# Optimization experiments

Hardware: AMD Instinct MI355X
Metric: run time of the kernel (lower is better)

## Reference

```python
import jax, jax.numpy as jnp
import numpy as np

NUM_SKILLS = 1000
DIM_S = 64
SIZE_M = 64
B, T = 64, 200


def setup_inputs() -> dict:
    key = jax.random.key(0)
    ks = jax.random.split(key, 16)
    skills = jax.random.randint(ks[0], (B, T), 0, NUM_SKILLS)
    responses = jax.random.randint(ks[1], (B, T), 0, 2)
    s = 1.0 / np.sqrt(DIM_S)
    return {
        "skills": skills,
        "responses": responses,
        "k_emb": jax.random.normal(ks[2], (NUM_SKILLS, DIM_S)) * s,
        "v_emb": jax.random.normal(ks[3], (2 * NUM_SKILLS, DIM_S)) * s,
        "Mk": jax.random.normal(ks[4], (SIZE_M, DIM_S)) * np.sqrt(2.0 / DIM_S),
        "Mv0": jax.random.normal(ks[5], (SIZE_M, DIM_S)) * np.sqrt(2.0 / DIM_S),
        "fW": jax.random.normal(ks[6], (DIM_S, 2 * DIM_S)) * (1.0 / np.sqrt(2 * DIM_S)),
        "fb": jnp.zeros((DIM_S,)),
        "eW": jax.random.normal(ks[7], (DIM_S, DIM_S)) * s,
        "eb": jnp.zeros((DIM_S,)),
        "aW": jax.random.normal(ks[8], (DIM_S, DIM_S)) * s,
        "ab": jnp.zeros((DIM_S,)),
        "pW": jax.random.normal(ks[9], (1, DIM_S)) * s,
        "pb": jnp.zeros((1,)),
    }


def reference(skills, responses, k_emb, v_emb, Mk, Mv0, fW, fb, eW, eb, aW, ab, pW, pb):
    # dropout is identity in eval mode
    masked_r = responses * (responses > -1).astype(responses.dtype)
    x = skills + NUM_SKILLS * masked_r            # [B, T]
    k = k_emb[skills]                              # [B, T, D]
    v = v_emb[x]                                   # [B, T, D]
    w = jax.nn.softmax(jnp.einsum('btd,md->btm', k, Mk), axis=-1)  # [B, T, M]
    e = jax.nn.sigmoid(v @ eW.T + eb)              # [B, T, D]
    a = jnp.tanh(v @ aW.T + ab)                    # [B, T, D]

    Mv_init = jnp.broadcast_to(Mv0, (skills.shape[0],) + Mv0.shape)  # [B, M, D]

    def step(Mvt, inp):
        wt, et, at = inp                           # [B,M], [B,D], [B,D]
        read = jnp.einsum('bm,bmd->bd', wt, Mvt)   # read BEFORE update (Mv[:, :-1])
        Mvt = Mvt * (1.0 - wt[:, :, None] * et[:, None, :]) + wt[:, :, None] * at[:, None, :]
        return Mvt, read

    xs = (jnp.swapaxes(w, 0, 1), jnp.swapaxes(e, 0, 1), jnp.swapaxes(a, 0, 1))
    _, reads = jax.lax.scan(step, Mv_init, xs)     # reads: [T, B, D]
    reads = jnp.swapaxes(reads, 0, 1)              # [B, T, D]

    f = jnp.tanh(jnp.concatenate([reads, k], axis=-1) @ fW.T + fb)  # [B, T, D]
    p = jax.nn.sigmoid(f @ pW.T + pb)[..., 0]      # [B, T]
    return p[:, 1:]                                # pred, [B, T-1]
```

## Files before the change

### kernel.cpp

```cpp
#include <hip/hip_runtime.h>
#include <hip/hip_bf16.h>
#include <stdint.h>

#define NSK 1000
#define TT  200
#define BB  64
#define NROW (BB * TT)
#define NOUT (BB * (TT-1))
#define CH  8
#define RW  8

__device__ __forceinline__ float lane_bcast(float v, int l) {
  return __uint_as_float(__builtin_amdgcn_readlane(__float_as_uint(v), l));
}
__device__ __forceinline__ unsigned ulane_bcast(unsigned v, int l) {
  return __builtin_amdgcn_readlane(v, l);
}
__device__ __forceinline__ float frcp(float x) { return __builtin_amdgcn_rcpf(x); }
__device__ __forceinline__ float sigm(float x) { return frcp(1.f + __expf(-x)); }
__device__ __forceinline__ float tanh_fast(float x) {
  return fmaf(-2.f, frcp(1.f + __expf(2.f * x)), 1.f);
}

typedef _Float16 half2v __attribute__((ext_vector_type(2)));
union H2U { unsigned u; half2v h; };
__device__ __forceinline__ unsigned pack2h(float a, float b) {
  H2U x; x.h = (half2v){(_Float16)a, (_Float16)b}; return x.u;
}
__device__ __forceinline__ float dot2h(unsigned sp, unsigned wp, float acc) {
#if __has_builtin(__builtin_amdgcn_fdot2)
  H2U s, w; s.u = sp; w.u = wp;
  return __builtin_amdgcn_fdot2(s.h, w.h, acc, false);
#else
  H2U s, w; s.u = sp; w.u = wp;
  return fmaf((float)s.h.y, (float)w.h.y, fmaf((float)s.h.x, (float)w.h.x, acc));
#endif
}
__device__ __forceinline__ unsigned pack_pairs(float v) {
  const int lane = threadIdx.x & 63;
  float a = __shfl(v, 2 * lane);
  float b = __shfl(v, 2 * lane + 1);
  return pack2h(a, b);
}

__global__ __launch_bounds__(256) void wea_kernel(
    const int* __restrict__ skills, const int* __restrict__ responses,
    const float* __restrict__ k_emb, const float* __restrict__ v_emb,
    const float* __restrict__ Mk, const float* __restrict__ eW,
    const float* __restrict__ eb, const float* __restrict__ aW,
    const float* __restrict__ ab,
    float* __restrict__ w_ws, float* __restrict__ e_ws, float* __restrict__ a_ws)
{
  __shared__ unsigned sw[3 * 64 * 40];
  const int tid = threadIdx.x;
  for (int ch = tid; ch < 1536; ch += 256) {
    const int mat = ch >> 9;
    const int rem = ch & 511;
    const int j = rem >> 3, cc = rem & 7;
    const float4* src = (mat == 0) ? (const float4*)Mk
                      : (mat == 1) ? (const float4*)eW : (const float4*)aW;
    const float4 f0 = src[j * 16 + cc * 2];
    const float4 f1 = src[j * 16 + cc * 2 + 1];
    uint4 pk;
    pk.x = pack2h(f0.x, f0.y); pk.y = pack2h(f0.z, f0.w);
    pk.z = pack2h(f1.x, f1.y); pk.w = pack2h(f1.z, f1.w);
    *(uint4*)&sw[mat * 2560 + j * 40 + ((cc + j) & 7) * 4] = pk;
  }
  __syncthreads();

  const int wave = tid >> 6, lane = tid & 63;
  const float ebl = eb[lane], abl = ab[lane];
  const int r0 = (blockIdx.x * 4 + wave) * 2;

  float kv[2], vv[2];
  #pragma unroll
  for (int i = 0; i < 2; ++i) {
    const int sk = skills[r0 + i];
    int rr = responses[r0 + i]; rr = (rr > -1) ? rr : 0;
    kv[i] = k_emb[(size_t)sk * 64 + lane];
    vv[i] = v_emb[(size_t)(sk + NSK * rr) * 64 + lane];
  }
  unsigned kp[2], vp[2];
  #pragma unroll
  for (int i = 0; i < 2; ++i) { kp[i] = pack_pairs(kv[i]); vp[i] = pack_pairs(vv[i]); }

  float accK[2] = {0.f, 0.f}, accE[2] = {0.f, 0.f}, accA[2] = {0.f, 0.f};
  #pragma unroll 1
  for (int h = 0; h < 2; ++h) {
    uint4 qm[4], qe[4], qa[4];
    #pragma unroll
    for (int c = 0; c < 4; ++c) {
      const int off = lane * 40 + (((h * 4 + c) + lane) & 7) * 4;
      qm[c] = *(const uint4*)&sw[off];
      qe[c] = *(const uint4*)&sw[2560 + off];
      qa[c] = *(const uint4*)&sw[5120 + off];
    }
    #pragma unroll
    for (int i = 0; i < 2; ++i) {
      #pragma unroll
      for (int c = 0; c < 4; ++c) {
        const unsigned um[4] = {qm[c].x, qm[c].y, qm[c].z, qm[c].w};
        const unsigned ue[4] = {qe[c].x, qe[c].y, qe[c].z, qe[c].w};
        const unsigned ua[4] = {qa[c].x, qa[c].y, qa[c].z, qa[c].w};
        #pragma unroll
        for (int m = 0; m < 4; ++m) {
          const int idx = (h * 4 + c) * 4 + m;
          const unsigned spk = ulane_bcast(kp[i], idx);
          const unsigned spv = ulane_bcast(vp[i], idx);
          accK[i] = dot2h(spk, um[m], accK[i]);
          accE[i] = dot2h(spv, ue[m], accE[i]);
          accA[i] = dot2h(spv, ua[m], accA[i]);
        }
      }
    }
  }

  #pragma unroll
  for (int i = 0; i < 2; ++i) {
    const int row = r0 + i;
    float mx = accK[i];
    #pragma unroll
    for (int off = 32; off; off >>= 1) mx = fmaxf(mx, __shfl_xor(mx, off));
    float ex = __expf(accK[i] - mx);
    float sm = ex;
    #pragma unroll
    for (int off = 32; off; off >>= 1) sm += __shfl_xor(sm, off);
    w_ws[(size_t)row * 64 + lane] = ex * frcp(sm);
    e_ws[(size_t)row * 64 + lane] = sigm(accE[i] + ebl);
    a_ws[(size_t)row * 64 + lane] = tanh_fast(accA[i] + abl);
  }
}

__device__ __forceinline__ void load_chunk(
    const float* __restrict__ wr, const float* __restrict__ er,
    const float* __restrict__ ar, int t0, int wl, int lane,
    float* wb, float* ebf, float* abf)
{
  #pragma unroll
  for (int k = 0; k < CH; ++k) {
    wb[k]  = wr[(t0 + k) * 64 + wl];
    ebf[k] = er[(t0 + k) * 64 + lane];
    abf[k] = ar[(t0 + k) * 64 + lane];
  }
}

__device__ __forceinline__ void compute_chunk(
    float* Mv, const float* wb, const float* ebf, const float* abf,
    float* __restrict__ red, int wave, int lane)
{
  #pragma unroll
  for (int k = 0; k < CH; ++k) {
    const float wv = wb[k], ev = ebf[k], av = abf[k];
    float rp = 0.f;
    #pragma unroll
    for (int i = 0; i < RW; ++i) {
      float wm = lane_bcast(wv, i);
      rp = fmaf(wm, Mv[i], rp);
      float tp = fmaf(-ev, Mv[i], av);
      Mv[i] = fmaf(wm, tp, Mv[i]);
    }
    red[k * 256 + wave * 64 + lane] = rp;
  }
}

__device__ __forceinline__ void reduce_store(
    const float* __restrict__ red, int ch, int b, int s, int wave, int lane,
    float* __restrict__ part_ws)
{
  #pragma unroll
  for (int u = 0; u < 2; ++u) {
    const float* rr = red + (wave * 2 + u) * 256;
    const float v = (rr[lane] + rr[64 + lane]) + (rr[128 + lane] + rr[192 + lane]);
    const int t = ch * CH + wave * 2 + u;
    part_ws[((size_t)b * TT + t) * 128 + s * 64 + lane] = v;
  }
}

__global__ __launch_bounds__(256) void scan_kernel(
    const float* __restrict__ Mv0,
    const float* __restrict__ w_ws, const float* __restrict__ e_ws,
    const float* __restrict__ a_ws, float* __restrict__ part_ws)
{
  __shared__ float red[2][CH * 256];
  const int b    = blockIdx.x >> 1;
  const int s    = blockIdx.x & 1;
  const int wave = threadIdx.x >> 6;
  const int lane = threadIdx.x & 63;
  const int m0   = s * 32 + wave * RW;
  const int wl   = m0 + (lane & (RW - 1));
  float Mv[RW];
  #pragma unroll
  for (int i = 0; i < RW; ++i) Mv[i] = Mv0[(size_t)(m0 + i) * 64 + lane];

  const float* wr = w_ws + (size_t)b * TT * 64;
  const float* er = e_ws + (size_t)b * TT * 64;
  const float* ar = a_ws + (size_t)b * TT * 64;

  float wb0[CH], eb0[CH], ab0[CH];
  float wb1[CH], eb1[CH], ab1[CH];
  load_chunk(wr, er, ar, 0, wl, lane, wb0, eb0, ab0);
  for (int ch = 0; ch < TT / CH; ch += 2) {
    if ((ch + 1) * CH < TT)
      load_chunk(wr, er, ar, (ch + 1) * CH, wl, lane, wb1, eb1, ab1);
    compute_chunk(Mv, wb0, eb0, ab0, red[0], wave, lane);
    __syncthreads();
    reduce_store(red[0], ch, b, s, wave, lane, part_ws);
    if ((ch + 2) * CH < TT)
      load_chunk(wr, er, ar, (ch + 2) * CH, wl, lane, wb0, eb0, ab0);
    if ((ch + 1) * CH < TT) {
      compute_chunk(Mv, wb1, eb1, ab1, red[1], wave, lane);
      __syncthreads();
      reduce_store(red[1], ch + 1, b, s, wave, lane, part_ws);
    }
  }
}

__global__ __launch_bounds__(256) void fp_kernel(
    const int* __restrict__ skills, const float* __restrict__ k_emb,
    const float* __restrict__ fW, const float* __restrict__ fb,
    const float* __restrict__ pW, const float* __restrict__ pb,
    const float* __restrict__ part_ws, float* __restrict__ out)
{
  __shared__ unsigned sf[64 * 72];
  const int tid = threadIdx.x;
  for (int ch = tid; ch < 1024; ch += 256) {
    const int j = ch >> 4, cc = ch & 15;
    const float4 f0 = ((const float4*)fW)[j * 32 + cc * 2];
    const float4 f1 = ((const float4*)fW)[j * 32 + cc * 2 + 1];
    uint4 pk;
    pk.x = pack2h(f0.x, f0.y); pk.y = pack2h(f0.z, f0.w);
    pk.z = pack2h(f1.x, f1.y); pk.w = pack2h(f1.z, f1.w);
    *(uint4*)&sf[j * 72 + ((cc + j) & 15) * 4] = pk;
  }
  __syncthreads();

  const int wave = tid >> 6, lane = tid & 63;
  const float fbl = fb[lane], pwl = pW[lane], pb0 = pb[0];
  const int p = blockIdx.x * 4 + wave;

  float pc[2][2], kc[2];
  int bsave[2], tsave[2];
  #pragma unroll
  for (int i = 0; i < 2; ++i) {
    const unsigned idx = 2u * p + i;
    const unsigned b = idx / 199u;
    const int row = (int)(idx + b + 1u);
    bsave[i] = (int)b; tsave[i] = (int)(idx - b * 199u);
    const float* pp = part_ws + (size_t)row * 128;
    pc[i][0] = pp[lane]; pc[i][1] = pp[64 + lane];
    kc[i] = k_emb[(size_t)skills[row] * 64 + lane];
  }
  unsigned rvp[2], kvp[2];
  #pragma unroll
  for (int i = 0; i < 2; ++i) {
    rvp[i] = pack_pairs(pc[i][0] + pc[i][1]);
    kvp[i] = pack_pairs(kc[i]);
  }

  float acc[2] = {fbl, fbl};
  #pragma unroll 1
  for (int h = 0; h < 4; ++h) {
    uint4 qf[4];
    #pragma unroll
    for (int c = 0; c < 4; ++c)
      qf[c] = *(const uint4*)&sf[lane * 72 + (((h * 4 + c) + lane) & 15) * 4];
    #pragma unroll
    for (int i = 0; i < 2; ++i) {
      #pragma unroll
      for (int c = 0; c < 4; ++c) {
        const unsigned uu[4] = {qf[c].x, qf[c].y, qf[c].z, qf[c].w};
        #pragma unroll
        for (int m = 0; m < 4; ++m) {
          const int idx = (h * 4 + c) * 4 + m;
          const unsigned sp = (idx < 32) ? ulane_bcast(rvp[i], idx)
                                         : ulane_bcast(kvp[i], idx - 32);
          acc[i] = dot2h(sp, uu[m], acc[i]);
        }
      }
    }
  }

  float f0 = tanh_fast(acc[0]) * pwl;
  float f1 = tanh_fast(acc[1]) * pwl;
  #pragma unroll
  for (int off = 32; off; off >>= 1) {
    f0 += __shfl_xor(f0, off);
    f1 += __shfl_xor(f1, off);
  }
  if (lane == 0) {
    out[(size_t)bsave[0] * (TT - 1) + tsave[0]] = sigm(f0 + pb0);
    out[(size_t)bsave[1] * (TT - 1) + tsave[1]] = sigm(f1 + pb0);
  }
}

extern "C" void kernel_launch(void* const* d_in, const int* in_sizes, int n_in,
                              void* d_out, int out_size, void* d_ws, size_t ws_size,
                              hipStream_t stream) {
  const int* skills    = (const int*)d_in[0];
  const int* responses = (const int*)d_in[1];
  const float* k_emb   = (const float*)d_in[2];
  const float* v_emb   = (const float*)d_in[3];
  const float* Mk      = (const float*)d_in[4];
  const float* Mv0     = (const float*)d_in[5];
  const float* fW      = (const float*)d_in[6];
  const float* fb      = (const float*)d_in[7];
  const float* eW      = (const float*)d_in[8];
  const float* eb      = (const float*)d_in[9];
  const float* aW      = (const float*)d_in[10];
  const float* ab      = (const float*)d_in[11];
  const float* pW      = (const float*)d_in[12];
  const float* pb      = (const float*)d_in[13];

  float* w_ws    = (float*)d_ws;
  float* e_ws    = w_ws + (size_t)BB * TT * 64;
  float* a_ws    = e_ws + (size_t)BB * TT * 64;
  float* part_ws = a_ws + (size_t)BB * TT * 64;

  wea_kernel<<<dim3(NROW / 8), 256, 0, stream>>>(
      skills, responses, k_emb, v_emb, Mk, eW, eb, aW, ab, w_ws, e_ws, a_ws);
  scan_kernel<<<dim3(BB * 2), 256, 0, stream>>>(Mv0, w_ws, e_ws, a_ws, part_ws);
  fp_kernel<<<dim3(NOUT / 8), 256, 0, stream>>>(
      skills, k_emb, fW, fb, pW, pb, part_ws, (float*)d_out);
}
```

Measured before the change: 135.2 us.

## Fuse three stages into one persistent kernel with per-batch atomic counters

Merges the projection, recurrent scan and output-projection kernels into a single launch whose blocks are split by role: 800 blocks produce w/e/a and bump per-batch counters, 128 scan blocks spin on those counters, and the first 796 producer blocks later wait on scan counters to compute outputs. This removes two kernel launch boundaries and lets scans for finished batches start while other batches are still being projected. Each producer block now handles 16 rows instead of 8. It risks deadlock if scan blocks are resident while producers cannot be scheduled, and adds a memset plus spin-wait overhead.

```diff
diff --git a/kernel.cpp b/kernel.cpp
--- a/kernel.cpp
+++ b/kernel.cpp
@@ -9,6 +9,10 @@
 #define NOUT (BB * (TT-1))
 #define CH  8
 #define RW  8
+#define NW  800
+#define NS  128
+#define NFP 796
+#define NBLK (NW + NS)
 
 __device__ __forceinline__ float lane_bcast(float v, int l) {
   return __uint_as_float(__builtin_amdgcn_readlane(__float_as_uint(v), l));
@@ -43,92 +47,9 @@
   return pack2h(a, b);
 }
 
-__global__ __launch_bounds__(256) void wea_kernel(
-    const int* __restrict__ skills, const int* __restrict__ responses,
-    const float* __restrict__ k_emb, const float* __restrict__ v_emb,
-    const float* __restrict__ Mk, const float* __restrict__ eW,
-    const float* __restrict__ eb, const float* __restrict__ aW,
-    const float* __restrict__ ab,
-    float* __restrict__ w_ws, float* __restrict__ e_ws, float* __restrict__ a_ws)
-{
-  __shared__ unsigned sw[3 * 64 * 40];
-  const int tid = threadIdx.x;
-  for (int ch = tid; ch < 1536; ch += 256) {
-    const int mat = ch >> 9;
-    const int rem = ch & 511;
-    const int j = rem >> 3, cc = rem & 7;
-    const float4* src = (mat == 0) ? (const float4*)Mk
-                      : (mat == 1) ? (const float4*)eW : (const float4*)aW;
-    const float4 f0 = src[j * 16 + cc * 2];
-    const float4 f1 = src[j * 16 + cc * 2 + 1];
-    uint4 pk;
-    pk.x = pack2h(f0.x, f0.y); pk.y = pack2h(f0.z, f0.w);
-    pk.z = pack2h(f1.x, f1.y); pk.w = pack2h(f1.z, f1.w);
-    *(uint4*)&sw[mat * 2560 + j * 40 + ((cc + j) & 7) * 4] = pk;
-  }
-  __syncthreads();
-
-  const int wave = tid >> 6, lane = tid & 63;
-  const float ebl = eb[lane], abl = ab[lane];
-  const int r0 = (blockIdx.x * 4 + wave) * 2;
-
-  float kv[2], vv[2];
-  #pragma unroll
-  for (int i = 0; i < 2; ++i) {
-    const int sk = skills[r0 + i];
-    int rr = responses[r0 + i]; rr = (rr > -1) ? rr : 0;
-    kv[i] = k_emb[(size_t)sk * 64 + lane];
-    vv[i] = v_emb[(size_t)(sk + NSK * rr) * 64 + lane];
-  }
-  unsigned kp[2], vp[2];
-  #pragma unroll
-  for (int i = 0; i < 2; ++i) { kp[i] = pack_pairs(kv[i]); vp[i] = pack_pairs(vv[i]); }
-
-  float accK[2] = {0.f, 0.f}, accE[2] = {0.f, 0.f}, accA[2] = {0.f, 0.f};
-  #pragma unroll 1
-  for (int h = 0; h < 2; ++h) {
-    uint4 qm[4], qe[4], qa[4];
-    #pragma unroll
-    for (int c = 0; c < 4; ++c) {
-      const int off = lane * 40 + (((h * 4 + c) + lane) & 7) * 4;
-      qm[c] = *(const uint4*)&sw[off];
-      qe[c] = *(const uint4*)&sw[2560 + off];
-      qa[c] = *(const uint4*)&sw[5120 + off];
-    }
-    #pragma unroll
-    for (int i = 0; i < 2; ++i) {
-      #pragma unroll
-      for (int c = 0; c < 4; ++c) {
-        const unsigned um[4] = {qm[c].x, qm[c].y, qm[c].z, qm[c].w};
-        const unsigned ue[4] = {qe[c].x, qe[c].y, qe[c].z, qe[c].w};
-        const unsigned ua[4] = {qa[c].x, qa[c].y, qa[c].z, qa[c].w};
-        #pragma unroll
-        for (int m = 0; m < 4; ++m) {
-          const int idx = (h * 4 + c) * 4 + m;
-          const unsigned spk = ulane_bcast(kp[i], idx);
-          const unsigned spv = ulane_bcast(vp[i], idx);
-          accK[i] = dot2h(spk, um[m], accK[i]);
-          accE[i] = dot2h(spv, ue[m], accE[i]);
-          accA[i] = dot2h(spv, ua[m], accA[i]);
-        }
-      }
-    }
-  }
-
-  #pragma unroll
-  for (int i = 0; i < 2; ++i) {
-    const int row = r0 + i;
-    float mx = accK[i];
-    #pragma unroll
-    for (int off = 32; off; off >>= 1) mx = fmaxf(mx, __shfl_xor(mx, off));
-    float ex = __expf(accK[i] - mx);
-    float sm = ex;
-    #pragma unroll
-    for (int off = 32; off; off >>= 1) sm += __shfl_xor(sm, off);
-    w_ws[(size_t)row * 64 + lane] = ex * frcp(sm);
-    e_ws[(size_t)row * 64 + lane] = sigm(accE[i] + ebl);
-    a_ws[(size_t)row * 64 + lane] = tanh_fast(accA[i] + abl);
-  }
+__device__ __forceinline__ void spin_ge(unsigned* p, unsigned tgt) {
+  while (__hip_atomic_load(p, __ATOMIC_RELAXED, __HIP_MEMORY_SCOPE_AGENT) < tgt)
+    __builtin_amdgcn_s_sleep(8);
 }
 
 __device__ __forceinline__ void load_chunk(
@@ -176,120 +97,230 @@
   }
 }
 
-__global__ __launch_bounds__(256) void scan_kernel(
-    const float* __restrict__ Mv0,
-    const float* __restrict__ w_ws, const float* __restrict__ e_ws,
-    const float* __restrict__ a_ws, float* __restrict__ part_ws)
+__global__ __launch_bounds__(256, 4) void dkvmn_pipe(
+    const int* __restrict__ skills, const int* __restrict__ responses,
+    const float* __restrict__ k_emb, const float* __restrict__ v_emb,
+    const float* __restrict__ Mk, const float* __restrict__ Mv0,
+    const float* __restrict__ fW, const float* __restrict__ fb,
+    const float* __restrict__ eW, const float* __restrict__ eb,
+    const float* __restrict__ aW, const float* __restrict__ ab,
+    const float* __restrict__ pW, const float* __restrict__ pb,
+    unsigned* __restrict__ wcnt, unsigned* __restrict__ scnt,
+    float* __restrict__ w_ws, float* __restrict__ e_ws, float* __restrict__ a_ws,
+    float* __restrict__ part_ws, float* __restrict__ out)
 {
-  __shared__ float red[2][CH * 256];
-  const int b    = blockIdx.x >> 1;
-  const int s    = blockIdx.x & 1;
-  const int wave = threadIdx.x >> 6;
-  const int lane = threadIdx.x & 63;
-  const int m0   = s * 32 + wave * RW;
-  const int wl   = m0 + (lane & (RW - 1));
-  float Mv[RW];
-  #pragma unroll
-  for (int i = 0; i < RW; ++i) Mv[i] = Mv0[(size_t)(m0 + i) * 64 + lane];
-
-  const float* wr = w_ws + (size_t)b * TT * 64;
-  const float* er = e_ws + (size_t)b * TT * 64;
-  const float* ar = a_ws + (size_t)b * TT * 64;
-
-  float wb0[CH], eb0[CH], ab0[CH];
-  float wb1[CH], eb1[CH], ab1[CH];
-  load_chunk(wr, er, ar, 0, wl, lane, wb0, eb0, ab0);
-  for (int ch = 0; ch < TT / CH; ch += 2) {
-    if ((ch + 1) * CH < TT)
-      load_chunk(wr, er, ar, (ch + 1) * CH, wl, lane, wb1, eb1, ab1);
-    compute_chunk(Mv, wb0, eb0, ab0, red[0], wave, lane);
+  __shared__ unsigned smem[7680];
+  const int tid = threadIdx.x;
+  const int wave = tid >> 6, lane = tid & 63;
+
+  if (blockIdx.x >= NW) {
+    const int j = blockIdx.x - NW, b = j >> 1, s = j & 1;
+    if (tid == 0) { spin_ge(&wcnt[b], 200u); __threadfence(); }
     __syncthreads();
-    reduce_store(red[0], ch, b, s, wave, lane, part_ws);
-    if ((ch + 2) * CH < TT)
-      load_chunk(wr, er, ar, (ch + 2) * CH, wl, lane, wb0, eb0, ab0);
-    if ((ch + 1) * CH < TT) {
-      compute_chunk(Mv, wb1, eb1, ab1, red[1], wave, lane);
+
+    const int m0 = s * 32 + wave * RW;
+    const int wl = m0 + (lane & (RW - 1));
+    float Mv[RW];
+    #pragma unroll
+    for (int i = 0; i < RW; ++i) Mv[i] = Mv0[(size_t)(m0 + i) * 64 + lane];
+
+    const float* wr = w_ws + (size_t)b * TT * 64;
+    const float* er = e_ws + (size_t)b * TT * 64;
+    const float* ar = a_ws + (size_t)b * TT * 64;
+    float* red0 = (float*)smem;
+    float* red1 = red0 + CH * 256;
+
+    float wb0[CH], eb0[CH], ab0[CH];
+    float wb1[CH], eb1[CH], ab1[CH];
+    load_chunk(wr, er, ar, 0, wl, lane, wb0, eb0, ab0);
+    for (int ch = 0; ch < TT / CH; ch += 2) {
+      if ((ch + 1) * CH < TT)
+        load_chunk(wr, er, ar, (ch + 1) * CH, wl, lane, wb1, eb1, ab1);
+      compute_chunk(Mv, wb0, eb0, ab0, red0, wave, lane);
       __syncthreads();
-      reduce_store(red[1], ch + 1, b, s, wave, lane, part_ws);
-    }
-  }
-}
-
-__global__ __launch_bounds__(256) void fp_kernel(
-    const int* __restrict__ skills, const float* __restrict__ k_emb,
-    const float* __restrict__ fW, const float* __restrict__ fb,
-    const float* __restrict__ pW, const float* __restrict__ pb,
-    const float* __restrict__ part_ws, float* __restrict__ out)
-{
-  __shared__ unsigned sf[64 * 72];
-  const int tid = threadIdx.x;
-  for (int ch = tid; ch < 1024; ch += 256) {
-    const int j = ch >> 4, cc = ch & 15;
-    const float4 f0 = ((const float4*)fW)[j * 32 + cc * 2];
-    const float4 f1 = ((const float4*)fW)[j * 32 + cc * 2 + 1];
+      reduce_store(red0, ch, b, s, wave, lane, part_ws);
+      if ((ch + 2) * CH < TT)
+        load_chunk(wr, er, ar, (ch + 2) * CH, wl, lane, wb0, eb0, ab0);
+      if ((ch + 1) * CH < TT) {
+        compute_chunk(Mv, wb1, eb1, ab1, red1, wave, lane);
+        __syncthreads();
+        reduce_store(red1, ch + 1, b, s, wave, lane, part_ws);
+      }
+    }
+    __syncthreads();
+    if (tid == 0) {
+      __threadfence();
+      __hip_atomic_fetch_add(&scnt[b], 1u, __ATOMIC_RELEASE, __HIP_MEMORY_SCOPE_AGENT);
+    }
+    return;
+  }
+
+  for (int ch = tid; ch < 1536; ch += 256) {
+    const int mat = ch >> 9, rem = ch & 511;
+    const int j = rem >> 3, cc = rem & 7;
+    const float4* src = (mat == 0) ? (const float4*)Mk
+                      : (mat == 1) ? (const float4*)eW : (const float4*)aW;
+    const float4 f0 = src[j * 16 + cc * 2];
+    const float4 f1 = src[j * 16 + cc * 2 + 1];
     uint4 pk;
     pk.x = pack2h(f0.x, f0.y); pk.y = pack2h(f0.z, f0.w);
     pk.z = pack2h(f1.x, f1.y); pk.w = pack2h(f1.z, f1.w);
-    *(uint4*)&sf[j * 72 + ((cc + j) & 15) * 4] = pk;
+    *(uint4*)&smem[mat * 2560 + j * 40 + ((cc + j) & 7) * 4] = pk;
   }
   __syncthreads();
-
-  const int wave = tid >> 6, lane = tid & 63;
-  const float fbl = fb[lane], pwl = pW[lane], pb0 = pb[0];
-  const int p = blockIdx.x * 4 + wave;
-
-  float pc[2][2], kc[2];
-  int bsave[2], tsave[2];
-  #pragma unroll
-  for (int i = 0; i < 2; ++i) {
-    const unsigned idx = 2u * p + i;
-    const unsigned b = idx / 199u;
-    const int row = (int)(idx + b + 1u);
-    bsave[i] = (int)b; tsave[i] = (int)(idx - b * 199u);
-    const float* pp = part_ws + (size_t)row * 128;
-    pc[i][0] = pp[lane]; pc[i][1] = pp[64 + lane];
-    kc[i] = k_emb[(size_t)skills[row] * 64 + lane];
-  }
-  unsigned rvp[2], kvp[2];
-  #pragma unroll
-  for (int i = 0; i < 2; ++i) {
-    rvp[i] = pack_pairs(pc[i][0] + pc[i][1]);
-    kvp[i] = pack_pairs(kc[i]);
-  }
-
-  float acc[2] = {fbl, fbl};
-  #pragma unroll 1
-  for (int h = 0; h < 4; ++h) {
-    uint4 qf[4];
-    #pragma unroll
-    for (int c = 0; c < 4; ++c)
-      qf[c] = *(const uint4*)&sf[lane * 72 + (((h * 4 + c) + lane) & 15) * 4];
-    #pragma unroll
-    for (int i = 0; i < 2; ++i) {
+  {
+    const float ebl = eb[lane], abl = ab[lane];
+    const int r0 = blockIdx.x * 16 + wave * 4;
+
+    float kv[4], vv[4];
+    #pragma unroll
+    for (int i = 0; i < 4; ++i) {
+      const int sk = skills[r0 + i];
+      int rr = responses[r0 + i]; rr = (rr > -1) ? rr : 0;
+      kv[i] = k_emb[(size_t)sk * 64 + lane];
+      vv[i] = v_emb[(size_t)(sk + NSK * rr) * 64 + lane];
+    }
+    unsigned kp[4], vp[4];
+    #pragma unroll
+    for (int i = 0; i < 4; ++i) { kp[i] = pack_pairs(kv[i]); vp[i] = pack_pairs(vv[i]); }
+
+    float accK[4] = {0,0,0,0}, accE[4] = {0,0,0,0}, accA[4] = {0,0,0,0};
+    #pragma unroll 1
+    for (int h = 0; h < 2; ++h) {
+      uint4 qm[4], qe[4], qa[4];
       #pragma unroll
       for (int c = 0; c < 4; ++c) {
-        const unsigned uu[4] = {qf[c].x, qf[c].y, qf[c].z, qf[c].w};
+        const int off = lane * 40 + (((h * 4 + c) + lane) & 7) * 4;
+        qm[c] = *(const uint4*)&smem[off];
+        qe[c] = *(const uint4*)&smem[2560 + off];
+        qa[c] = *(const uint4*)&smem[5120 + off];
+      }
+      #pragma unroll
+      for (int i = 0; i < 4; ++i) {
         #pragma unroll
-        for (int m = 0; m < 4; ++m) {
-          const int idx = (h * 4 + c) * 4 + m;
-          const unsigned sp = (idx < 32) ? ulane_bcast(rvp[i], idx)
-                                         : ulane_bcast(kvp[i], idx - 32);
-          acc[i] = dot2h(sp, uu[m], acc[i]);
+        for (int c = 0; c < 4; ++c) {
+          const unsigned um[4] = {qm[c].x, qm[c].y, qm[c].z, qm[c].w};
+          const unsigned ue[4] = {qe[c].x, qe[c].y, qe[c].z, qe[c].w};
+          const unsigned ua[4] = {qa[c].x, qa[c].y, qa[c].z, qa[c].w};
+          #pragma unroll
+          for (int m = 0; m < 4; ++m) {
+            const int idx = (h * 4 + c) * 4 + m;
+            const unsigned spk = ulane_bcast(kp[i], idx);
+            const unsigned spv = ulane_bcast(vp[i], idx);
+            accK[i] = dot2h(spk, um[m], accK[i]);
+            accE[i] = dot2h(spv, ue[m], accE[i]);
+            accA[i] = dot2h(spv, ua[m], accA[i]);
+          }
         }
       }
     }
-  }
-
-  float f0 = tanh_fast(acc[0]) * pwl;
-  float f1 = tanh_fast(acc[1]) * pwl;
-  #pragma unroll
-  for (int off = 32; off; off >>= 1) {
-    f0 += __shfl_xor(f0, off);
-    f1 += __shfl_xor(f1, off);
-  }
-  if (lane == 0) {
-    out[(size_t)bsave[0] * (TT - 1) + tsave[0]] = sigm(f0 + pb0);
-    out[(size_t)bsave[1] * (TT - 1) + tsave[1]] = sigm(f1 + pb0);
+    #pragma unroll
+    for (int i = 0; i < 4; ++i) {
+      const int row = r0 + i;
+      float mx = accK[i];
+      #pragma unroll
+      for (int off = 32; off; off >>= 1) mx = fmaxf(mx, __shfl_xor(mx, off));
+      float ex = __expf(accK[i] - mx);
+      float sm = ex;
+      #pragma unroll
+      for (int off = 32; off; off >>= 1) sm += __shfl_xor(sm, off);
+      w_ws[(size_t)row * 64 + lane] = ex * frcp(sm);
+      e_ws[(size_t)row * 64 + lane] = sigm(accE[i] + ebl);
+      a_ws[(size_t)row * 64 + lane] = tanh_fast(accA[i] + abl);
+    }
+  }
+  __syncthreads();
+  if (tid == 0) {
+    __threadfence();
+    const int r0 = blockIdx.x * 16;
+    const int b0 = r0 / TT, b1 = (r0 + 15) / TT;
+    if (b0 == b1) {
+      __hip_atomic_fetch_add(&wcnt[b0], 16u, __ATOMIC_RELEASE, __HIP_MEMORY_SCOPE_AGENT);
+    } else {
+      const unsigned n0 = (unsigned)((b0 + 1) * TT - r0);
+      __hip_atomic_fetch_add(&wcnt[b0], n0, __ATOMIC_RELEASE, __HIP_MEMORY_SCOPE_AGENT);
+      __hip_atomic_fetch_add(&wcnt[b1], 16u - n0, __ATOMIC_RELEASE, __HIP_MEMORY_SCOPE_AGENT);
+    }
+  }
+
+  if (blockIdx.x >= NFP) return;
+
+  {
+    const int idx0 = blockIdx.x * 16, idx1 = idx0 + 15;
+    const int bf = idx0 / 199, bl = idx1 / 199;
+    if (tid == 0) {
+      spin_ge(&scnt[bf], 2u);
+      if (bl != bf) spin_ge(&scnt[bl], 2u);
+      __threadfence();
+    }
+    __syncthreads();
+    for (int ch = tid; ch < 1024; ch += 256) {
+      const int j = ch >> 4, cc = ch & 15;
+      const float4 f0 = ((const float4*)fW)[j * 32 + cc * 2];
+      const float4 f1 = ((const float4*)fW)[j * 32 + cc * 2 + 1];
+      uint4 pk;
+      pk.x = pack2h(f0.x, f0.y); pk.y = pack2h(f0.z, f0.w);
+      pk.z = pack2h(f1.x, f1.y); pk.w = pack2h(f1.z, f1.w);
+      *(uint4*)&smem[j * 72 + ((cc + j) & 15) * 4] = pk;
+    }
+    __syncthreads();
+
+    const float fbl = fb[lane], pwl = pW[lane], pb0 = pb[0];
+    #pragma unroll 1
+    for (int pi = 0; pi < 2; ++pi) {
+      const int p = blockIdx.x * 8 + wave * 2 + pi;
+      float pc[2][2], kc[2];
+      int bsave[2], tsave[2];
+      #pragma unroll
+      for (int i = 0; i < 2; ++i) {
+        const unsigned idx = 2u * p + i;
+        const unsigned b = idx / 199u;
+        const int row = (int)(idx + b + 1u);
+        bsave[i] = (int)b; tsave[i] = (int)(idx - b * 199u);
+        const float* pp = part_ws + (size_t)row * 128;
+        pc[i][0] = pp[lane]; pc[i][1] = pp[64 + lane];
+        kc[i] = k_emb[(size_t)skills[row] * 64 + lane];
+      }
+      unsigned rvp[2], kvp[2];
+      #pragma unroll
+      for (int i = 0; i < 2; ++i) {
+        rvp[i] = pack_pairs(pc[i][0] + pc[i][1]);
+        kvp[i] = pack_pairs(kc[i]);
+      }
+      float acc[2] = {fbl, fbl};
+      #pragma unroll 1
+      for (int h = 0; h < 4; ++h) {
+        uint4 qf[4];
+        #pragma unroll
+        for (int c = 0; c < 4; ++c)
+          qf[c] = *(const uint4*)&smem[lane * 72 + (((h * 4 + c) + lane) & 15) * 4];
+        #pragma unroll
+        for (int i = 0; i < 2; ++i) {
+          #pragma unroll
+          for (int c = 0; c < 4; ++c) {
+            const unsigned uu[4] = {qf[c].x, qf[c].y, qf[c].z, qf[c].w};
+            #pragma unroll
+            for (int m = 0; m < 4; ++m) {
+              const int idx = (h * 4 + c) * 4 + m;
+              const unsigned sp = (idx < 32) ? ulane_bcast(rvp[i], idx)
+                                             : ulane_bcast(kvp[i], idx - 32);
+              acc[i] = dot2h(sp, uu[m], acc[i]);
+            }
+          }
+        }
+      }
+      float f0 = tanh_fast(acc[0]) * pwl;
+      float f1 = tanh_fast(acc[1]) * pwl;
+      #pragma unroll
+      for (int off = 32; off; off >>= 1) {
+        f0 += __shfl_xor(f0, off);
+        f1 += __shfl_xor(f1, off);
+      }
+      if (lane == 0) {
+        out[(size_t)bsave[0] * (TT - 1) + tsave[0]] = sigm(f0 + pb0);
+        out[(size_t)bsave[1] * (TT - 1) + tsave[1]] = sigm(f1 + pb0);
+      }
+    }
   }
 }
 
@@ -311,14 +342,16 @@
   const float* pW      = (const float*)d_in[12];
   const float* pb      = (const float*)d_in[13];
 
-  float* w_ws    = (float*)d_ws;
+  unsigned* wcnt = (unsigned*)d_ws;
+  unsigned* scnt = wcnt + 64;
+  float* base    = (float*)d_ws + 256;
+  float* w_ws    = base;
   float* e_ws    = w_ws + (size_t)BB * TT * 64;
   float* a_ws    = e_ws + (size_t)BB * TT * 64;
   float* part_ws = a_ws + (size_t)BB * TT * 64;
 
-  wea_kernel<<<dim3(NROW / 8), 256, 0, stream>>>(
-      skills, responses, k_emb, v_emb, Mk, eW, eb, aW, ab, w_ws, e_ws, a_ws);
-  scan_kernel<<<dim3(BB * 2), 256, 0, stream>>>(Mv0, w_ws, e_ws, a_ws, part_ws);
-  fp_kernel<<<dim3(NOUT / 8), 256, 0, stream>>>(
-      skills, k_emb, fW, fb, pW, pb, part_ws, (float*)d_out);
-}
+  hipMemsetAsync(d_ws, 0, 1024, stream);
+  dkvmn_pipe<<<dim3(NBLK), dim3(256), 0, stream>>>(
+      skills, responses, k_emb, v_emb, Mk, Mv0, fW, fb, eW, eb, aW, ab, pW, pb,
+      wcnt, scnt, w_ws, e_ws, a_ws, part_ws, (float*)d_out);
+}
```

Measured after the change: 207.7 us. +53.6%, slower.

## Fuse memory scan and output projection into one per-batch kernel

Applied to the files above, without the earlier changes.

Merges the scan kernel and the final projection kernel into a single kernel with one 512-thread block per batch row. Each block holds all 64 memory slots, so the cross-block partial-read sum goes away, and the block then runs the fW/pW projection over its own reads. This drops a kernel launch and the partial-sum round trip, but cuts the scan grid from 128 to 64 blocks. The projection phase is also limited to 64 blocks, which lowers parallelism on a GPU with many compute units.

```diff
diff --git a/kernel.cpp b/kernel.cpp
--- a/kernel.cpp
+++ b/kernel.cpp
@@ -6,7 +6,6 @@
 #define TT  200
 #define BB  64
 #define NROW (BB * TT)
-#define NOUT (BB * (TT-1))
 #define CH  8
 #define RW  8
 
@@ -54,8 +53,7 @@
   __shared__ unsigned sw[3 * 64 * 40];
   const int tid = threadIdx.x;
   for (int ch = tid; ch < 1536; ch += 256) {
-    const int mat = ch >> 9;
-    const int rem = ch & 511;
+    const int mat = ch >> 9, rem = ch & 511;
     const int j = rem >> 3, cc = rem & 7;
     const float4* src = (mat == 0) ? (const float4*)Mk
                       : (mat == 1) ? (const float4*)eW : (const float4*)aW;
@@ -114,7 +112,6 @@
       }
     }
   }
-
   #pragma unroll
   for (int i = 0; i < 2; ++i) {
     const int row = r0 + i;
@@ -159,137 +156,113 @@
       float tp = fmaf(-ev, Mv[i], av);
       Mv[i] = fmaf(wm, tp, Mv[i]);
     }
-    red[k * 256 + wave * 64 + lane] = rp;
-  }
-}
-
-__device__ __forceinline__ void reduce_store(
-    const float* __restrict__ red, int ch, int b, int s, int wave, int lane,
-    float* __restrict__ part_ws)
-{
-  #pragma unroll
-  for (int u = 0; u < 2; ++u) {
-    const float* rr = red + (wave * 2 + u) * 256;
-    const float v = (rr[lane] + rr[64 + lane]) + (rr[128 + lane] + rr[192 + lane]);
-    const int t = ch * CH + wave * 2 + u;
-    part_ws[((size_t)b * TT + t) * 128 + s * 64 + lane] = v;
-  }
-}
-
-__global__ __launch_bounds__(256) void scan_kernel(
+    red[k * 512 + wave * 64 + lane] = rp;
+  }
+}
+
+__global__ __launch_bounds__(512) void sfp_kernel(
+    const int* __restrict__ skills, const float* __restrict__ k_emb,
     const float* __restrict__ Mv0,
-    const float* __restrict__ w_ws, const float* __restrict__ e_ws,
-    const float* __restrict__ a_ws, float* __restrict__ part_ws)
-{
-  __shared__ float red[2][CH * 256];
-  const int b    = blockIdx.x >> 1;
-  const int s    = blockIdx.x & 1;
-  const int wave = threadIdx.x >> 6;
-  const int lane = threadIdx.x & 63;
-  const int m0   = s * 32 + wave * RW;
-  const int wl   = m0 + (lane & (RW - 1));
-  float Mv[RW];
-  #pragma unroll
-  for (int i = 0; i < RW; ++i) Mv[i] = Mv0[(size_t)(m0 + i) * 64 + lane];
-
-  const float* wr = w_ws + (size_t)b * TT * 64;
-  const float* er = e_ws + (size_t)b * TT * 64;
-  const float* ar = a_ws + (size_t)b * TT * 64;
-
-  float wb0[CH], eb0[CH], ab0[CH];
-  float wb1[CH], eb1[CH], ab1[CH];
-  load_chunk(wr, er, ar, 0, wl, lane, wb0, eb0, ab0);
-  for (int ch = 0; ch < TT / CH; ch += 2) {
-    if ((ch + 1) * CH < TT)
-      load_chunk(wr, er, ar, (ch + 1) * CH, wl, lane, wb1, eb1, ab1);
-    compute_chunk(Mv, wb0, eb0, ab0, red[0], wave, lane);
-    __syncthreads();
-    reduce_store(red[0], ch, b, s, wave, lane, part_ws);
-    if ((ch + 2) * CH < TT)
-      load_chunk(wr, er, ar, (ch + 2) * CH, wl, lane, wb0, eb0, ab0);
-    if ((ch + 1) * CH < TT) {
-      compute_chunk(Mv, wb1, eb1, ab1, red[1], wave, lane);
-      __syncthreads();
-      reduce_store(red[1], ch + 1, b, s, wave, lane, part_ws);
-    }
-  }
-}
-
-__global__ __launch_bounds__(256) void fp_kernel(
-    const int* __restrict__ skills, const float* __restrict__ k_emb,
     const float* __restrict__ fW, const float* __restrict__ fb,
     const float* __restrict__ pW, const float* __restrict__ pb,
-    const float* __restrict__ part_ws, float* __restrict__ out)
-{
-  __shared__ unsigned sf[64 * 72];
+    const float* __restrict__ w_ws, const float* __restrict__ e_ws,
+    const float* __restrict__ a_ws,
+    float* __restrict__ read_ws, float* __restrict__ out)
+{
+  __shared__ float sred[2][CH * 512];
+  __shared__ unsigned sfw[64 * 72];
   const int tid = threadIdx.x;
-  for (int ch = tid; ch < 1024; ch += 256) {
+  const int wave = tid >> 6, lane = tid & 63;
+  const int b = blockIdx.x, base = b * TT;
+
+  for (int ch = tid; ch < 1024; ch += 512) {
     const int j = ch >> 4, cc = ch & 15;
     const float4 f0 = ((const float4*)fW)[j * 32 + cc * 2];
     const float4 f1 = ((const float4*)fW)[j * 32 + cc * 2 + 1];
     uint4 pk;
     pk.x = pack2h(f0.x, f0.y); pk.y = pack2h(f0.z, f0.w);
     pk.z = pack2h(f1.x, f1.y); pk.w = pack2h(f1.z, f1.w);
-    *(uint4*)&sf[j * 72 + ((cc + j) & 15) * 4] = pk;
-  }
+    *(uint4*)&sfw[j * 72 + ((cc + j) & 15) * 4] = pk;
+  }
+
+  const int m0 = wave * RW;
+  const int wl = m0 + (lane & (RW - 1));
+  float Mv[RW];
+  #pragma unroll
+  for (int i = 0; i < RW; ++i) Mv[i] = Mv0[(size_t)(m0 + i) * 64 + lane];
+  const float* wr = w_ws + (size_t)base * 64;
+  const float* er = e_ws + (size_t)base * 64;
+  const float* ar = a_ws + (size_t)base * 64;
+
+  float wb0[CH], eb0[CH], ab0[CH];
+  float wb1[CH], eb1[CH], ab1[CH];
+  load_chunk(wr, er, ar, 0, wl, lane, wb0, eb0, ab0);
   __syncthreads();
 
-  const int wave = tid >> 6, lane = tid & 63;
+  for (int c = 0; c < TT / CH; ++c) {
+    if (c + 1 < TT / CH) {
+      if (c & 1) load_chunk(wr, er, ar, (c + 1) * CH, wl, lane, wb0, eb0, ab0);
+      else       load_chunk(wr, er, ar, (c + 1) * CH, wl, lane, wb1, eb1, ab1);
+    }
+    float* red = sred[c & 1];
+    if (c & 1) compute_chunk(Mv, wb1, eb1, ab1, red, wave, lane);
+    else       compute_chunk(Mv, wb0, eb0, ab0, red, wave, lane);
+    __syncthreads();
+    const float* r = red + wave * 512;
+    float v = ((r[0 * 64 + lane] + r[1 * 64 + lane]) + (r[2 * 64 + lane] + r[3 * 64 + lane]))
+            + ((r[4 * 64 + lane] + r[5 * 64 + lane]) + (r[6 * 64 + lane] + r[7 * 64 + lane]));
+    read_ws[(size_t)(base + c * CH + wave) * 64 + lane] = v;
+  }
+  __threadfence_block();
+  __syncthreads();
+
   const float fbl = fb[lane], pwl = pW[lane], pb0 = pb[0];
-  const int p = blockIdx.x * 4 + wave;
-
-  float pc[2][2], kc[2];
-  int bsave[2], tsave[2];
-  #pragma unroll
-  for (int i = 0; i < 2; ++i) {
-    const unsigned idx = 2u * p + i;
-    const unsigned b = idx / 199u;
-    const int row = (int)(idx + b + 1u);
-    bsave[i] = (int)b; tsave[i] = (int)(idx - b * 199u);
-    const float* pp = part_ws + (size_t)row * 128;
-    pc[i][0] = pp[lane]; pc[i][1] = pp[64 + lane];
-    kc[i] = k_emb[(size_t)skills[row] * 64 + lane];
-  }
-  unsigned rvp[2], kvp[2];
-  #pragma unroll
-  for (int i = 0; i < 2; ++i) {
-    rvp[i] = pack_pairs(pc[i][0] + pc[i][1]);
-    kvp[i] = pack_pairs(kc[i]);
-  }
-
-  float acc[2] = {fbl, fbl};
   #pragma unroll 1
-  for (int h = 0; h < 4; ++h) {
-    uint4 qf[4];
-    #pragma unroll
-    for (int c = 0; c < 4; ++c)
-      qf[c] = *(const uint4*)&sf[lane * 72 + (((h * 4 + c) + lane) & 15) * 4];
-    #pragma unroll
-    for (int i = 0; i < 2; ++i) {
-      #pragma unroll
-      for (int c = 0; c < 4; ++c) {
-        const unsigned uu[4] = {qf[c].x, qf[c].y, qf[c].z, qf[c].w};
+  for (int g0 = 0; g0 < 25; g0 += 5) {
+    float rv[5], kc[5];
+    int ov[5];
+    #pragma unroll
+    for (int i = 0; i < 5; ++i) {
+      const int o = wave * 25 + g0 + i;
+      ov[i] = o;
+      const int t = (o < TT - 1) ? o + 1 : TT - 1;
+      rv[i] = read_ws[(size_t)(base + t) * 64 + lane];
+      kc[i] = k_emb[(size_t)skills[base + t] * 64 + lane];
+    }
+    unsigned rvp[5], kvp[5];
+    #pragma unroll
+    for (int i = 0; i < 5; ++i) { rvp[i] = pack_pairs(rv[i]); kvp[i] = pack_pairs(kc[i]); }
+
+    float acc[5] = {fbl, fbl, fbl, fbl, fbl};
+    #pragma unroll 1
+    for (int h = 0; h < 4; ++h) {
+      uint4 qf[4];
+      #pragma unroll
+      for (int c = 0; c < 4; ++c)
+        qf[c] = *(const uint4*)&sfw[lane * 72 + (((h * 4 + c) + lane) & 15) * 4];
+      #pragma unroll
+      for (int i = 0; i < 5; ++i) {
         #pragma unroll
-        for (int m = 0; m < 4; ++m) {
-          const int idx = (h * 4 + c) * 4 + m;
-          const unsigned sp = (idx < 32) ? ulane_bcast(rvp[i], idx)
-                                         : ulane_bcast(kvp[i], idx - 32);
-          acc[i] = dot2h(sp, uu[m], acc[i]);
+        for (int c = 0; c < 4; ++c) {
+          const unsigned uu[4] = {qf[c].x, qf[c].y, qf[c].z, qf[c].w};
+          #pragma unroll
+          for (int m = 0; m < 4; ++m) {
+            const int idx = (h * 4 + c) * 4 + m;
+            const unsigned sp = (idx < 32) ? ulane_bcast(rvp[i], idx)
+                                           : ulane_bcast(kvp[i], idx - 32);
+            acc[i] = dot2h(sp, uu[m], acc[i]);
+          }
         }
       }
     }
-  }
-
-  float f0 = tanh_fast(acc[0]) * pwl;
-  float f1 = tanh_fast(acc[1]) * pwl;
-  #pragma unroll
-  for (int off = 32; off; off >>= 1) {
-    f0 += __shfl_xor(f0, off);
-    f1 += __shfl_xor(f1, off);
-  }
-  if (lane == 0) {
-    out[(size_t)bsave[0] * (TT - 1) + tsave[0]] = sigm(f0 + pb0);
-    out[(size_t)bsave[1] * (TT - 1) + tsave[1]] = sigm(f1 + pb0);
+    #pragma unroll
+    for (int i = 0; i < 5; ++i) {
+      float f = tanh_fast(acc[i]) * pwl;
+      #pragma unroll
+      for (int off = 32; off; off >>= 1) f += __shfl_xor(f, off);
+      if (lane == 0 && ov[i] < TT - 1)
+        out[(size_t)b * (TT - 1) + ov[i]] = sigm(f + pb0);
+    }
   }
 }
 
@@ -314,11 +287,11 @@
   float* w_ws    = (float*)d_ws;
   float* e_ws    = w_ws + (size_t)BB * TT * 64;
   float* a_ws    = e_ws + (size_t)BB * TT * 64;
-  float* part_ws = a_ws + (size_t)BB * TT * 64;
+  float* read_ws = a_ws + (size_t)BB * TT * 64;
 
   wea_kernel<<<dim3(NROW / 8), 256, 0, stream>>>(
       skills, responses, k_emb, v_emb, Mk, eW, eb, aW, ab, w_ws, e_ws, a_ws);
-  scan_kernel<<<dim3(BB * 2), 256, 0, stream>>>(Mv0, w_ws, e_ws, a_ws, part_ws);
-  fp_kernel<<<dim3(NOUT / 8), 256, 0, stream>>>(
-      skills, k_emb, fW, fb, pW, pb, part_ws, (float*)d_out);
-}
+  sfp_kernel<<<dim3(BB), 512, 0, stream>>>(
+      skills, k_emb, Mv0, fW, fb, pW, pb, w_ws, e_ws, a_ws,
+      read_ws, (float*)d_out);
+}
```

Measured after the change: 198.4 us. 1.47x slower.

## Store intermediates as fp16 and enlarge scan chunk to cut memory traffic

Applied to the files above, without the earlier changes.

The w/e/a workspaces are now written in half precision, with e and a packed together into one 32-bit word and w in 16-bit. The scan's partial read outputs are split into two fp16 arrays, one per half-block. The scan chunk size grows from 8 to 20 timesteps, so there are fewer barriers and the loads are prefetched in larger batches. The aim is to shrink global-memory traffic between kernels and the synchronisation count in the serial scan. The costs are lower precision in the recurrence inputs and outputs, higher register pressure from the larger chunk buffers, and more shared memory.

```diff
diff --git a/kernel.cpp b/kernel.cpp
--- a/kernel.cpp
+++ b/kernel.cpp
@@ -7,7 +7,7 @@
 #define BB  64
 #define NROW (BB * TT)
 #define NOUT (BB * (TT-1))
-#define CH  8
+#define CH  20
 #define RW  8
 
 __device__ __forceinline__ float lane_bcast(float v, int l) {
@@ -26,6 +26,15 @@
 union H2U { unsigned u; half2v h; };
 __device__ __forceinline__ unsigned pack2h(float a, float b) {
   H2U x; x.h = (half2v){(_Float16)a, (_Float16)b}; return x.u;
+}
+__device__ __forceinline__ unsigned short f16bits(float x) {
+  H2U u; u.h = (half2v){(_Float16)x, (_Float16)0.f}; return (unsigned short)(u.u & 0xffffu);
+}
+__device__ __forceinline__ float f16lo(unsigned bits) {
+  H2U u; u.u = bits; return (float)u.h.x;
+}
+__device__ __forceinline__ float f16hi(unsigned bits) {
+  H2U u; u.u = bits; return (float)u.h.y;
 }
 __device__ __forceinline__ float dot2h(unsigned sp, unsigned wp, float acc) {
 #if __has_builtin(__builtin_amdgcn_fdot2)
@@ -49,13 +58,12 @@
     const float* __restrict__ Mk, const float* __restrict__ eW,
     const float* __restrict__ eb, const float* __restrict__ aW,
     const float* __restrict__ ab,
-    float* __restrict__ w_ws, float* __restrict__ e_ws, float* __restrict__ a_ws)
+    unsigned* __restrict__ ea_ws, unsigned short* __restrict__ w16_ws)
 {
   __shared__ unsigned sw[3 * 64 * 40];
   const int tid = threadIdx.x;
   for (int ch = tid; ch < 1536; ch += 256) {
-    const int mat = ch >> 9;
-    const int rem = ch & 511;
+    const int mat = ch >> 9, rem = ch & 511;
     const int j = rem >> 3, cc = rem & 7;
     const float4* src = (mat == 0) ? (const float4*)Mk
                       : (mat == 1) ? (const float4*)eW : (const float4*)aW;
@@ -114,7 +122,6 @@
       }
     }
   }
-
   #pragma unroll
   for (int i = 0; i < 2; ++i) {
     const int row = r0 + i;
@@ -125,36 +132,36 @@
     float sm = ex;
     #pragma unroll
     for (int off = 32; off; off >>= 1) sm += __shfl_xor(sm, off);
-    w_ws[(size_t)row * 64 + lane] = ex * frcp(sm);
-    e_ws[(size_t)row * 64 + lane] = sigm(accE[i] + ebl);
-    a_ws[(size_t)row * 64 + lane] = tanh_fast(accA[i] + abl);
+    const float wv  = ex * frcp(sm);
+    const float evv = sigm(accE[i] + ebl);
+    const float avv = tanh_fast(accA[i] + abl);
+    ea_ws[(size_t)row * 64 + lane]  = pack2h(evv, avv);
+    w16_ws[(size_t)row * 64 + lane] = f16bits(wv);
   }
 }
 
 __device__ __forceinline__ void load_chunk(
-    const float* __restrict__ wr, const float* __restrict__ er,
-    const float* __restrict__ ar, int t0, int wl, int lane,
-    float* wb, float* ebf, float* abf)
+    const unsigned* __restrict__ eap, const unsigned short* __restrict__ wp,
+    int t0, int wl, int lane, unsigned* eab, unsigned* wvb)
 {
   #pragma unroll
   for (int k = 0; k < CH; ++k) {
-    wb[k]  = wr[(t0 + k) * 64 + wl];
-    ebf[k] = er[(t0 + k) * 64 + lane];
-    abf[k] = ar[(t0 + k) * 64 + lane];
+    eab[k] = eap[(t0 + k) * 64 + lane];
+    wvb[k] = (unsigned)wp[(t0 + k) * 64 + wl];
   }
 }
 
 __device__ __forceinline__ void compute_chunk(
-    float* Mv, const float* wb, const float* ebf, const float* abf,
+    float* Mv, const unsigned* eab, const unsigned* wvb,
     float* __restrict__ red, int wave, int lane)
 {
   #pragma unroll
   for (int k = 0; k < CH; ++k) {
-    const float wv = wb[k], ev = ebf[k], av = abf[k];
+    const float ev = f16lo(eab[k]), av = f16hi(eab[k]);
     float rp = 0.f;
     #pragma unroll
     for (int i = 0; i < RW; ++i) {
-      float wm = lane_bcast(wv, i);
+      const float wm = f16lo(ulane_bcast(wvb[k], i));
       rp = fmaf(wm, Mv[i], rp);
       float tp = fmaf(-ev, Mv[i], av);
       Mv[i] = fmaf(wm, tp, Mv[i]);
@@ -164,53 +171,54 @@
 }
 
 __device__ __forceinline__ void reduce_store(
-    const float* __restrict__ red, int ch, int b, int s, int wave, int lane,
-    float* __restrict__ part_ws)
-{
-  #pragma unroll
-  for (int u = 0; u < 2; ++u) {
-    const float* rr = red + (wave * 2 + u) * 256;
+    const float* __restrict__ red, int ch, int base, int wave, int lane,
+    unsigned short* __restrict__ ps)
+{
+  #pragma unroll
+  for (int u = 0; u < 5; ++u) {
+    const int k = wave * 5 + u;
+    const float* rr = red + k * 256;
     const float v = (rr[lane] + rr[64 + lane]) + (rr[128 + lane] + rr[192 + lane]);
-    const int t = ch * CH + wave * 2 + u;
-    part_ws[((size_t)b * TT + t) * 128 + s * 64 + lane] = v;
+    ps[(size_t)(base + ch * CH + k) * 64 + lane] = f16bits(v);
   }
 }
 
 __global__ __launch_bounds__(256) void scan_kernel(
     const float* __restrict__ Mv0,
-    const float* __restrict__ w_ws, const float* __restrict__ e_ws,
-    const float* __restrict__ a_ws, float* __restrict__ part_ws)
+    const unsigned* __restrict__ ea_ws, const unsigned short* __restrict__ w16_ws,
+    unsigned short* __restrict__ p0, unsigned short* __restrict__ p1)
 {
   __shared__ float red[2][CH * 256];
   const int b    = blockIdx.x >> 1;
   const int s    = blockIdx.x & 1;
   const int wave = threadIdx.x >> 6;
   const int lane = threadIdx.x & 63;
+  const int base = b * TT;
   const int m0   = s * 32 + wave * RW;
   const int wl   = m0 + (lane & (RW - 1));
+  unsigned short* ps = s ? p1 : p0;
+
   float Mv[RW];
   #pragma unroll
   for (int i = 0; i < RW; ++i) Mv[i] = Mv0[(size_t)(m0 + i) * 64 + lane];
 
-  const float* wr = w_ws + (size_t)b * TT * 64;
-  const float* er = e_ws + (size_t)b * TT * 64;
-  const float* ar = a_ws + (size_t)b * TT * 64;
-
-  float wb0[CH], eb0[CH], ab0[CH];
-  float wb1[CH], eb1[CH], ab1[CH];
-  load_chunk(wr, er, ar, 0, wl, lane, wb0, eb0, ab0);
+  const unsigned* eap = ea_ws + (size_t)base * 64;
+  const unsigned short* wp = w16_ws + (size_t)base * 64;
+
+  unsigned ea0[CH], wv0[CH], ea1[CH], wv1[CH];
+  load_chunk(eap, wp, 0, wl, lane, ea0, wv0);
   for (int ch = 0; ch < TT / CH; ch += 2) {
     if ((ch + 1) * CH < TT)
-      load_chunk(wr, er, ar, (ch + 1) * CH, wl, lane, wb1, eb1, ab1);
-    compute_chunk(Mv, wb0, eb0, ab0, red[0], wave, lane);
+      load_chunk(eap, wp, (ch + 1) * CH, wl, lane, ea1, wv1);
+    compute_chunk(Mv, ea0, wv0, red[0], wave, lane);
     __syncthreads();
-    reduce_store(red[0], ch, b, s, wave, lane, part_ws);
+    reduce_store(red[0], ch, base, wave, lane, ps);
     if ((ch + 2) * CH < TT)
-      load_chunk(wr, er, ar, (ch + 2) * CH, wl, lane, wb0, eb0, ab0);
+      load_chunk(eap, wp, (ch + 2) * CH, wl, lane, ea0, wv0);
     if ((ch + 1) * CH < TT) {
-      compute_chunk(Mv, wb1, eb1, ab1, red[1], wave, lane);
+      compute_chunk(Mv, ea1, wv1, red[1], wave, lane);
       __syncthreads();
-      reduce_store(red[1], ch + 1, b, s, wave, lane, part_ws);
+      reduce_store(red[1], ch + 1, base, wave, lane, ps);
     }
   }
 }
@@ -219,7 +227,8 @@
     const int* __restrict__ skills, const float* __restrict__ k_emb,
     const float* __restrict__ fW, const float* __restrict__ fb,
     const float* __restrict__ pW, const float* __restrict__ pb,
-    const float* __restrict__ part_ws, float* __restrict__ out)
+    const unsigned short* __restrict__ p0, const unsigned short* __restrict__ p1,
+    float* __restrict__ out)
 {
   __shared__ unsigned sf[64 * 72];
   const int tid = threadIdx.x;
@@ -238,7 +247,7 @@
   const float fbl = fb[lane], pwl = pW[lane], pb0 = pb[0];
   const int p = blockIdx.x * 4 + wave;
 
-  float pc[2][2], kc[2];
+  float rv[2], kc[2];
   int bsave[2], tsave[2];
   #pragma unroll
   for (int i = 0; i < 2; ++i) {
@@ -246,14 +255,14 @@
     const unsigned b = idx / 199u;
     const int row = (int)(idx + b + 1u);
     bsave[i] = (int)b; tsave[i] = (int)(idx - b * 199u);
-    const float* pp = part_ws + (size_t)row * 128;
-    pc[i][0] = pp[lane]; pc[i][1] = pp[64 + lane];
+    rv[i] = f16lo((unsigned)p0[(size_t)row * 64 + lane])
+          + f16lo((unsigned)p1[(size_t)row * 64 + lane]);
     kc[i] = k_emb[(size_t)skills[row] * 64 + lane];
   }
   unsigned rvp[2], kvp[2];
   #pragma unroll
   for (int i = 0; i < 2; ++i) {
-    rvp[i] = pack_pairs(pc[i][0] + pc[i][1]);
+    rvp[i] = pack_pairs(rv[i]);
     kvp[i] = pack_pairs(kc[i]);
   }
 
@@ -311,14 +320,14 @@
   const float* pW      = (const float*)d_in[12];
   const float* pb      = (const float*)d_in[13];
 
-  float* w_ws    = (float*)d_ws;
-  float* e_ws    = w_ws + (size_t)BB * TT * 64;
-  float* a_ws    = e_ws + (size_t)BB * TT * 64;
-  float* part_ws = a_ws + (size_t)BB * TT * 64;
+  unsigned* ea_ws       = (unsigned*)d_ws;
+  unsigned short* w16_ws = (unsigned short*)(ea_ws + (size_t)NROW * 64);
+  unsigned short* p0    = w16_ws + (size_t)NROW * 64;
+  unsigned short* p1    = p0 + (size_t)NROW * 64;
 
   wea_kernel<<<dim3(NROW / 8), 256, 0, stream>>>(
-      skills, responses, k_emb, v_emb, Mk, eW, eb, aW, ab, w_ws, e_ws, a_ws);
-  scan_kernel<<<dim3(BB * 2), 256, 0, stream>>>(Mv0, w_ws, e_ws, a_ws, part_ws);
+      skills, responses, k_emb, v_emb, Mk, eW, eb, aW, ab, ea_ws, w16_ws);
+  scan_kernel<<<dim3(BB * 2), 256, 0, stream>>>(Mv0, ea_ws, w16_ws, p0, p1);
   fp_kernel<<<dim3(NOUT / 8), 256, 0, stream>>>(
-      skills, k_emb, fW, fb, pW, pb, part_ws, (float*)d_out);
-}
+      skills, k_emb, fW, fb, pW, pb, p0, p1, (float*)d_out);
+}
```

Result: faster. 128.7 us (-4.8%).
